# Performance work log

Hardware: AMD Instinct MI355X
Metric: run time of the kernel (lower is better)

Reference implementation:

```python
import jax, jax.numpy as jnp
import numpy as np

K = 9
VOCAB = 7
DIM = 512
LOW = 256  # downsampled bottleneck dim
N_LAYERS = 2
EPS = 1e-5


def _inorm(x, g, b):
    # InstanceNorm1d over length axis (biased var), x: (N, C, K)
    m = jnp.mean(x, axis=-1, keepdims=True)
    v = jnp.mean((x - m) ** 2, axis=-1, keepdims=True)
    return g[None, :, None] * (x - m) * jax.lax.rsqrt(v + EPS) + b[None, :, None]


def _conv5_same(x, w, b):
    # x: (N, C, K), w: (O, C, 5), dilation 1, padding 'same' -> pad 2
    y = jax.lax.conv_general_dilated(
        x, w, window_strides=(1,), padding=[(2, 2)],
        dimension_numbers=('NCH', 'OIH', 'NCH'))
    return y + b[None, :, None]


def _bytenet_layer(x, p):
    (g1, b1, g2, b2, g3, b3, w1, c1b, w2, c2b, w3, c3b) = p
    h = jax.nn.gelu(_inorm(x, g1, b1), approximate=False)
    h = jnp.einsum('nck,oc->nok', h, w1) + c1b[None, :, None]      # 1x1 conv 512->256
    h = jax.nn.gelu(_inorm(h, g2, b2), approximate=False)
    h = _conv5_same(h, w2, c2b)                                     # k=5 conv 256->256
    h = jax.nn.gelu(_inorm(h, g3, b3), approximate=False)
    h = jnp.einsum('nck,oc->nok', h, w3) + c3b[None, :, None]      # 1x1 conv 256->512
    return h + x  # dropout is identity in eval


def setup_inputs() -> dict:
    key = jax.random.key(0)
    ks = jax.random.split(key, 16)
    x = jax.random.randint(ks[0], (8, 2048), 0, VOCAB)
    emb = jax.random.normal(ks[1], (VOCAB, DIM), jnp.float32) * 0.02
    emb = emb.at[6].set(0.0)  # padding_idx=6
    d = {
        'x': x,
        'emb': emb,
        'ln1_w': jnp.ones((N_LAYERS, DIM)), 'ln1_b': jnp.zeros((N_LAYERS, DIM)),
        'ln2_w': jnp.ones((N_LAYERS, LOW)), 'ln2_b': jnp.zeros((N_LAYERS, LOW)),
        'ln3_w': jnp.ones((N_LAYERS, LOW)), 'ln3_b': jnp.zeros((N_LAYERS, LOW)),
        'c1_w': jax.random.normal(ks[2], (N_LAYERS, LOW, DIM), jnp.float32) * 0.02,
        'c1_b': jnp.zeros((N_LAYERS, LOW)),
        'c2_w': jax.random.normal(ks[3], (N_LAYERS, LOW, LOW, 5), jnp.float32) * 0.02,
        'c2_b': jnp.zeros((N_LAYERS, LOW)),
        'c3_w': jax.random.normal(ks[4], (N_LAYERS, DIM, LOW), jnp.float32) * 0.02,
        'c3_b': jnp.zeros((N_LAYERS, DIM)),
        'out_w': jax.random.normal(ks[5], (VOCAB, DIM * K), jnp.float32) * 0.02,
        'out_b': jnp.zeros((VOCAB,)),
    }
    return d


def reference(x, emb, ln1_w, ln1_b, ln2_w, ln2_b, ln3_w, ln3_b,
              c1_w, c1_b, c2_w, c2_b, c3_w, c3_b, out_w, out_b):
    B, L = x.shape
    W = L - K + 1
    e = emb[x]                                        # (B, L, D)
    idx = jnp.arange(W)[:, None] + jnp.arange(K)      # (W, K)
    win = e[:, idx, :]                                # (B, W, K, D)
    h = win.transpose(0, 1, 3, 2).reshape(B * W, DIM, K)  # (N, D, K)
    for i in range(N_LAYERS):
        p = (ln1_w[i], ln1_b[i], ln2_w[i], ln2_b[i], ln3_w[i], ln3_b[i],
             c1_w[i], c1_b[i], c2_w[i], c2_b[i], c3_w[i], c3_b[i])
        h = _bytenet_layer(h, p)
    pred = h.reshape(B * W, DIM * K) @ out_w.T + out_b
    return pred.reshape(B, W, VOCAB)
```

## Files before the change

### kernel.cpp

```cpp
#include <hip/hip_runtime.h>

typedef __attribute__((ext_vector_type(8))) short bfv8;
typedef __attribute__((ext_vector_type(4))) float f32x4;
typedef __attribute__((ext_vector_type(4))) unsigned short usv4;

typedef __attribute__((address_space(1))) const void gvoid;
typedef __attribute__((address_space(3))) void lvoid;
__device__ __forceinline__ void gload16(const void* g, void* l) {
  __builtin_amdgcn_global_load_lds((gvoid*)g, (lvoid*)l, 16, 0, 0);
}

__device__ __forceinline__ float bf2f(unsigned short u) {
  union { unsigned int i; float f; } c; c.i = ((unsigned int)u) << 16; return c.f;
}
__device__ __forceinline__ unsigned short f2bf(float f) {
  union { float f; unsigned int i; } c; c.f = f;
  unsigned int r = c.i + 0x7FFFu + ((c.i >> 16) & 1u);
  return (unsigned short)(r >> 16);
}
__device__ __forceinline__ float gelu_(float x) {
  float z2 = 1.5957691216057308f * x * __builtin_fmaf(0.044715f, x * x, 1.0f);
  float e = __expf(z2);
  float t = __builtin_amdgcn_rcpf(e + 1.0f);
  return x - x * t;
}
__device__ __forceinline__ int div9(int col) {
  return (int)(__umulhi((unsigned)col, 954437177u) >> 1);
}

#define CHP 132

__global__ void k_prep(const float* c1w, const float* c2w, const float* c3w,
                       const float* outw, unsigned short* W1b, unsigned short* W2t,
                       unsigned short* W3b, float* OWt) {
  int i = blockIdx.x * 256 + threadIdx.x;
  if (i < 262144) { W1b[i] = f2bf(c1w[i]); return; }
  i -= 262144;
  if (i < 655360) {
    int ii = i & 255, o = (i >> 8) & 255, rest = i >> 16;
    int t = rest % 5, l = rest / 5;
    W2t[i] = f2bf(c2w[(((l * 256 + o) << 8) + ii) * 5 + t]);
    return;
  }
  i -= 655360;
  if (i < 262144) { W3b[i] = f2bf(c3w[i]); return; }
  i -= 262144;
  if (i < 32256) {
    int c = i & 511, rk = i >> 9;
    int r = rk / 9, k = rk - 9 * r;
    OWt[i] = outw[r * 4608 + c * 9 + k];
  }
}

__global__ void k_x0(const int* x, const float* emb, unsigned short* X, int n0) {
  int idx = blockIdx.x * 256 + threadIdx.x;
  int c4 = idx & 127, nl = idx >> 7;
  int gn = n0 + nl, b = gn >> 11, w = gn & 2047;
  unsigned short* dst = X + (size_t)(12 + nl * 12) * 512 + (c4 << 2);
  const int* xb = x + (b << 11);
  #pragma unroll
  for (int k = 0; k < 9; k++) {
    int t = w + k; if (t > 2047) t = 2047;
    const float* e = emb + xb[t] * 512 + (c4 << 2);
    float4 ev = *(const float4*)e;
    usv4 pk;
    pk[0] = f2bf(ev.x); pk[1] = f2bf(ev.y);
    pk[2] = f2bf(ev.z); pk[3] = f2bf(ev.w);
    *(usv4*)(dst + k * 512) = pk;
  }
}

__global__ void k_zpad(unsigned short* AL) {
  int i = threadIdx.x;
  for (; i < 12 * 256; i += 256) AL[i] = 0;
}

template <int MODE>
__global__ __launch_bounds__(512, 2) void k_gemm(
    const unsigned short* __restrict__ Aw, const unsigned short* __restrict__ Bsrc,
    const float* __restrict__ cbias, const float* __restrict__ n1w,
    const float* __restrict__ n1b, const float* __restrict__ gw,
    const float* __restrict__ gb, unsigned short* __restrict__ Out, int nkc) {
  __shared__ __align__(16) unsigned short smem[69632];
  unsigned short* sE = smem;

  const int KROW = (MODE == 0) ? 512 : 256;
  const int KSTEPS = (MODE == 1) ? 20 : ((MODE == 0) ? 8 : 4);
  int tid = threadIdx.x, wv = tid >> 6, ln = tid & 63;
  int lr = ln >> 3, lu = ln & 7;
  int swz = (lu ^ lr) << 3;
  int m0 = (MODE == 2) ? ((int)blockIdx.y << 8) : 0;
  int w0 = blockIdx.x << 5;
  int col0 = blockIdx.x * 288;

  int brow[5];
  #pragma unroll
  for (int s = 0; s < 5; s++) {
    int colg = col0 + (s << 6) + (wv << 3) + lr;
    if (colg >= nkc) colg = nkc - 1;
    brow[s] = colg + 3 * div9(colg) + 12;
  }
  const unsigned short* A0 = Aw + (size_t)m0 * KROW;

  f32x4 acc[4][9];
  #pragma unroll
  for (int i = 0; i < 4; i++)
    #pragma unroll
    for (int j = 0; j < 9; j++) acc[i][j] = (f32x4){0.f, 0.f, 0.f, 0.f};

  auto stage = [&](int buf, int ks) {
    int kb, dlt; const unsigned short* Ab;
    if (MODE == 1) {
      int t = ks % 5; kb = (ks / 5) << 6; dlt = t - 2; Ab = A0 + t * 65536;
    } else { kb = ks << 6; dlt = 0; Ab = A0; }
    unsigned short* cA = smem + buf * 16384;
    unsigned short* cB = smem + 32768 + buf * 18432;
    #pragma unroll
    for (int p = 0; p < 4; p++) {
      int m = (p << 6) + (wv << 3) + lr;
      gload16(Ab + (size_t)m * KROW + kb + swz, cA + (p << 12) + (wv << 9));
    }
    #pragma unroll
    for (int s = 0; s < 4; s++)
      gload16(Bsrc + (size_t)(brow[s] + dlt) * KROW + kb + swz,
              cB + (s << 12) + (wv << 9));
    if (wv < 4)
      gload16(Bsrc + (size_t)(brow[4] + dlt) * KROW + kb + swz,
              cB + (4 << 12) + (wv << 9));
  };

  stage(0, 0);
  __syncthreads();

  int cur = 0;
  for (int ks = 0; ks < KSTEPS; ks++) {
    unsigned short* cA = smem + cur * 16384;
    unsigned short* cB = smem + 32768 + cur * 18432;

    if (MODE == 0) {
      int cg = tid & 15, win = tid >> 4;
      int u = cg >> 1, sub = (cg & 1) << 3;
      int gch = (ks << 6) + (cg << 2);
      float v[9][4], s1[4] = {0.f, 0.f, 0.f, 0.f};
      #pragma unroll
      for (int k = 0; k < 9; k++) {
        int cl = win * 9 + k;
        usv4 rv = *(const usv4*)((char*)cB + cl * 128 + ((u ^ (cl & 7)) << 4) + sub);
        #pragma unroll
        for (int j = 0; j < 4; j++) { v[k][j] = bf2f(rv[j]); s1[j] += v[k][j]; }
      }
      float mn[4], rr[4], gg[4], bo[4];
      #pragma unroll
      for (int j = 0; j < 4; j++) {
        mn[j] = s1[j] * (1.0f / 9.0f);
        float q = 0.f;
        #pragma unroll
        for (int k = 0; k < 9; k++) { float d = v[k][j] - mn[j]; q += d * d; }
        rr[j] = rsqrtf(q * (1.0f / 9.0f) + 1e-5f);
        gg[j] = n1w[gch + j]; bo[j] = n1b[gch + j];
      }
      #pragma unroll
      for (int k = 0; k < 9; k++) {
        int cl = win * 9 + k;
        usv4 pk;
        #pragma unroll
        for (int j = 0; j < 4; j++)
          pk[j] = f2bf(gelu_(gg[j] * (v[k][j] - mn[j]) * rr[j] + bo[j]));
        *(usv4*)((char*)cB + cl * 128 + ((u ^ (cl & 7)) << 4) + sub) = pk;
      }
      __syncthreads();
    }

    if (ks + 1 < KSTEPS) stage(cur ^ 1, ks + 1);

    int l16 = ln & 15, loct = ln >> 4;
    int wm = wv >> 1, wn = wv & 1;
    #pragma unroll
    for (int kk = 0; kk < 2; kk++) {
      int kbyte = (kk << 6) + (loct << 4);
      bfv8 af[4], bf_[9];
      #pragma unroll
      for (int mi = 0; mi < 4; mi++) {
        int row = (wm << 6) + (mi << 4) + l16;
        af[mi] = *(const bfv8*)((const char*)cA + row * 128 + (kbyte ^ ((row & 7) << 4)));
      }
      #pragma unroll
      for (int ni = 0; ni < 9; ni++) {
        int row = wn * 144 + (ni << 4) + l16;
        bf_[ni] = *(const bfv8*)((const char*)cB + row * 128 + (kbyte ^ ((row & 7) << 4)));
      }
      #pragma unroll
      for (int mi = 0; mi < 4; mi++)
        #pragma unroll
        for (int ni = 0; ni < 9; ni++)
          acc[mi][ni] = __builtin_amdgcn_mfma_f32_16x16x32_bf16(
              af[mi], bf_[ni], acc[mi][ni], 0, 0, 0);
    }
    __syncthreads();
    cur ^= 1;
  }

  int l16 = ln & 15, loct = ln >> 4;
  #pragma unroll
  for (int R = 0; R < 2; R++) {
    if (R) __syncthreads();
    if ((wv >> 2) == R) {
      int chh = (((wv >> 1) & 1) << 6) + (loct << 2);
      int colb = (wv & 1) * 144 + l16;
      #pragma unroll
      for (int mi = 0; mi < 4; mi++) {
        #pragma unroll
        for (int ni = 0; ni < 9; ni++) {
          usv4 pk;
          #pragma unroll
          for (int q = 0; q < 4; q++) pk[q] = f2bf(acc[mi][ni][q]);
          *(usv4*)(sE + (colb + (ni << 4)) * CHP + chh + (mi << 4)) = pk;
        }
      }
    }
    __syncthreads();
    #pragma unroll
    for (int tt = 0; tt < 2; tt++) {
      int t = tid + tt * 512;
      int c4 = t & 31, win = t >> 5;
      int chl = (R << 7) + (c4 << 2);
      const unsigned short* sb = sE + (win * 9) * CHP + (c4 << 2);
      if (MODE == 2) {
        int chg = m0 + chl;
        size_t ob = (size_t)(12 + (size_t)(w0 + win) * 12) * 512 + chg;
        float cb[4];
        #pragma unroll
        for (int j = 0; j < 4; j++) cb[j] = cbias[chg + j];
        #pragma unroll
        for (int k = 0; k < 9; k++) {
          usv4 rv = *(const usv4*)(sb + k * CHP);
          usv4 old = *(usv4*)(Out + ob + k * 512);
          usv4 pk;
          #pragma unroll
          for (int j = 0; j < 4; j++)
            pk[j] = f2bf(bf2f(rv[j]) + cb[j] + bf2f(old[j]));
          *(usv4*)(Out + ob + k * 512) = pk;
        }
      } else {
        size_t ob = (size_t)(12 + (size_t)(w0 + win) * 12) * 256 + chl;
        float s1[4] = {0.f, 0.f, 0.f, 0.f}, s2[4] = {0.f, 0.f, 0.f, 0.f};
        #pragma unroll
        for (int k = 0; k < 9; k++) {
          usv4 rv = *(const usv4*)(sb + k * CHP);
          #pragma unroll
          for (int j = 0; j < 4; j++) {
            float f = bf2f(rv[j]);
            s1[j] += f; s2[j] = __builtin_fmaf(f, f, s2[j]);
          }
        }
        float mn[4], rr[4], gg[4], bo[4];
        #pragma unroll
        for (int j = 0; j < 4; j++) {
          mn[j] = s1[j] * (1.0f / 9.0f);
          float var = s2[j] * (1.0f / 9.0f) - mn[j] * mn[j];
          rr[j] = rsqrtf(var + 1e-5f);
          gg[j] = gw[chl + j]; bo[j] = gb[chl + j];
        }
        #pragma unroll
        for (int k = 0; k < 9; k++) {
          usv4 rv = *(const usv4*)(sb + k * CHP);
          usv4 pk;
          #pragma unroll
          for (int j = 0; j < 4; j++)
            pk[j] = f2bf(gelu_(gg[j] * (bf2f(rv[j]) - mn[j]) * rr[j] + bo[j]));
          *(usv4*)(Out + ob + k * 256) = pk;
        }
        if (MODE == 0) {
          usv4 z = (usv4){0, 0, 0, 0};
          *(usv4*)(Out + ob + 9 * 256) = z;
          *(usv4*)(Out + ob + 10 * 256) = z;
          *(usv4*)(Out + ob + 11 * 256) = z;
        }
      }
    }
  }
}

__global__ void k_out(const unsigned short* X, const float* OWt, const float* outb,
                      float* pred, int n0, int nc) {
  int gw = (blockIdx.x * 256 + threadIdx.x) >> 6;
  int ln = threadIdx.x & 63;
  if (gw >= nc) return;
  int gn = n0 + gw, b = gn >> 11, w = gn & 2047;
  if (w >= 2040) return;
  const unsigned short* xb = X + (size_t)(12 + gw * 12) * 512 + ln * 8;
  float a[7];
  #pragma unroll
  for (int r = 0; r < 7; r++) a[r] = 0.f;
  for (int k = 0; k < 9; k++) {
    bfv8 xv = *(const bfv8*)(xb + k * 512);
    float xf[8];
    #pragma unroll
    for (int j = 0; j < 8; j++) xf[j] = bf2f((unsigned short)xv[j]);
    #pragma unroll
    for (int r = 0; r < 7; r++) {
      const float* wp = OWt + (r * 9 + k) * 512 + ln * 8;
      float4 w0 = *(const float4*)(wp);
      float4 w1 = *(const float4*)(wp + 4);
      a[r] += xf[0] * w0.x + xf[1] * w0.y + xf[2] * w0.z + xf[3] * w0.w +
              xf[4] * w1.x + xf[5] * w1.y + xf[6] * w1.z + xf[7] * w1.w;
    }
  }
  #pragma unroll
  for (int r = 0; r < 7; r++)
    for (int off = 32; off; off >>= 1) a[r] += __shfl_down(a[r], off);
  if (ln == 0) {
    float* o = pred + (size_t)(b * 2040 + w) * 7;
    #pragma unroll
    for (int r = 0; r < 7; r++) o[r] = a[r] + outb[r];
  }
}

extern "C" void kernel_launch(void* const* d_in, const int* in_sizes, int n_in,
                              void* d_out, int out_size, void* d_ws, size_t ws_size,
                              hipStream_t stream) {
  const int*   x    = (const int*)d_in[0];
  const float* emb  = (const float*)d_in[1];
  const float* ln1w = (const float*)d_in[2];
  const float* ln1b = (const float*)d_in[3];
  const float* ln2w = (const float*)d_in[4];
  const float* ln2b = (const float*)d_in[5];
  const float* ln3w = (const float*)d_in[6];
  const float* ln3b = (const float*)d_in[7];
  const float* c1w  = (const float*)d_in[8];
  const float* c2w  = (const float*)d_in[10];
  const float* c3w  = (const float*)d_in[12];
  const float* c3b  = (const float*)d_in[13];
  const float* outw = (const float*)d_in[14];
  const float* outb = (const float*)d_in[15];
  float* pred = (float*)d_out;

  int nc = 8192;
  while (nc > 128 &&
         2488320ull + (unsigned long long)(nc + 1) * 24576ull > ws_size)
    nc >>= 1;
  int nkc = nc * 9;
  int tiles = nc >> 5;
  int nchunks = 16384 / nc;

  char* ws = (char*)d_ws;
  unsigned short* W1b = (unsigned short*)(ws);
  unsigned short* W2t = (unsigned short*)(ws + 524288);
  unsigned short* W3b = (unsigned short*)(ws + 1835008);
  float*          OWt = (float*)(ws + 2359296);
  char* act = ws + 2488320;
  size_t hiB = (size_t)(nc + 1) * 12288;
  size_t loB = (size_t)(nc + 1) * 6144;
  unsigned short* X   = (unsigned short*)(act);
  unsigned short* AL  = (unsigned short*)(act + hiB);
  unsigned short* AL2 = (unsigned short*)(act + hiB + loB);

  k_prep<<<(1211904 + 255) / 256, 256, 0, stream>>>(c1w, c2w, c3w, outw,
                                                    W1b, W2t, W3b, OWt);
  k_zpad<<<1, 256, 0, stream>>>(AL);

  for (int ch = 0; ch < nchunks; ch++) {
    int n0 = ch * nc;
    k_x0<<<nc / 2, 256, 0, stream>>>(x, emb, X, n0);
    for (int l = 0; l < 2; l++) {
      k_gemm<0><<<dim3(tiles, 1), 512, 0, stream>>>(
          W1b + l * 131072, X, nullptr, ln1w + l * 512, ln1b + l * 512,
          ln2w + l * 256, ln2b + l * 256, AL, nkc);
      k_gemm<1><<<dim3(tiles, 1), 512, 0, stream>>>(
          W2t + l * 327680, AL, nullptr, nullptr, nullptr,
          ln3w + l * 256, ln3b + l * 256, AL2, nkc);
      k_gemm<2><<<dim3(tiles, 2), 512, 0, stream>>>(
          W3b + l * 131072, AL2, c3b + l * 512, nullptr, nullptr,
          nullptr, nullptr, X, nkc);
    }
    k_out<<<nc / 4, 256, 0, stream>>>(X, OWt, outb, pred, n0, nc);
  }
}
```

Before: 798.0 us.

## Halve GEMM tile to 256x144 with 256 threads and single-buffered LDS

Shrinks the fused GEMM block tile from 288 columns (32 windows) to 144 columns (16 windows) and from 512 to 256 threads, doubling the grid. It drops the LDS double buffer and stages each k-step synchronously, cutting LDS use from about 136KB to about 50KB so more blocks fit per CU. The epilogue is reworked to four rounds of one wave each. The cost is that global loads no longer overlap with MFMA inside a block, and each block reuses the A tile across fewer columns.

```diff
diff --git a/kernel.cpp b/kernel.cpp
--- a/kernel.cpp
+++ b/kernel.cpp
@@ -28,7 +28,7 @@
   return (int)(__umulhi((unsigned)col, 954437177u) >> 1);
 }
 
-#define CHP 132
+#define CHP 66
 
 __global__ void k_prep(const float* c1w, const float* c2w, const float* c3w,
                        const float* outw, unsigned short* W1b, unsigned short* W2t,
@@ -76,31 +76,34 @@
 }
 
 template <int MODE>
-__global__ __launch_bounds__(512, 2) void k_gemm(
+__global__ __launch_bounds__(256, 2) void k_gemm(
     const unsigned short* __restrict__ Aw, const unsigned short* __restrict__ Bsrc,
     const float* __restrict__ cbias, const float* __restrict__ n1w,
     const float* __restrict__ n1b, const float* __restrict__ gw,
     const float* __restrict__ gb, unsigned short* __restrict__ Out, int nkc) {
-  __shared__ __align__(16) unsigned short smem[69632];
+  __shared__ __align__(16) unsigned short smem[25600];
+  unsigned short* cA = smem;
+  unsigned short* cB = smem + 16384;
   unsigned short* sE = smem;
 
   const int KROW = (MODE == 0) ? 512 : 256;
   const int KSTEPS = (MODE == 1) ? 20 : ((MODE == 0) ? 8 : 4);
   int tid = threadIdx.x, wv = tid >> 6, ln = tid & 63;
   int lr = ln >> 3, lu = ln & 7;
-  int swz = (lu ^ lr) << 3;
   int m0 = (MODE == 2) ? ((int)blockIdx.y << 8) : 0;
-  int w0 = blockIdx.x << 5;
-  int col0 = blockIdx.x * 288;
+  int w0 = blockIdx.x << 4;
+  int col0 = blockIdx.x * 144;
 
   int brow[5];
   #pragma unroll
   for (int s = 0; s < 5; s++) {
-    int colg = col0 + (s << 6) + (wv << 3) + lr;
+    int cl = (s < 4) ? ((s << 5) + (wv << 3) + lr) : (128 + (wv << 3) + lr);
+    int colg = col0 + cl;
     if (colg >= nkc) colg = nkc - 1;
     brow[s] = colg + 3 * div9(colg) + 12;
   }
   const unsigned short* A0 = Aw + (size_t)m0 * KROW;
+  int swz = (lu ^ lr) << 3;
 
   f32x4 acc[4][9];
   #pragma unroll
@@ -108,34 +111,26 @@
     #pragma unroll
     for (int j = 0; j < 9; j++) acc[i][j] = (f32x4){0.f, 0.f, 0.f, 0.f};
 
-  auto stage = [&](int buf, int ks) {
+  for (int ks = 0; ks < KSTEPS; ks++) {
     int kb, dlt; const unsigned short* Ab;
     if (MODE == 1) {
       int t = ks % 5; kb = (ks / 5) << 6; dlt = t - 2; Ab = A0 + t * 65536;
     } else { kb = ks << 6; dlt = 0; Ab = A0; }
-    unsigned short* cA = smem + buf * 16384;
-    unsigned short* cB = smem + 32768 + buf * 18432;
-    #pragma unroll
-    for (int p = 0; p < 4; p++) {
-      int m = (p << 6) + (wv << 3) + lr;
-      gload16(Ab + (size_t)m * KROW + kb + swz, cA + (p << 12) + (wv << 9));
+
+    if (ks) __syncthreads();
+    #pragma unroll
+    for (int p = 0; p < 8; p++) {
+      int m = (p << 5) + (wv << 3) + lr;
+      gload16(Ab + (size_t)m * KROW + kb + swz, cA + ((p << 5) + (wv << 3)) * 64);
     }
     #pragma unroll
     for (int s = 0; s < 4; s++)
       gload16(Bsrc + (size_t)(brow[s] + dlt) * KROW + kb + swz,
-              cB + (s << 12) + (wv << 9));
-    if (wv < 4)
+              cB + ((s << 5) + (wv << 3)) * 64);
+    if (wv < 2)
       gload16(Bsrc + (size_t)(brow[4] + dlt) * KROW + kb + swz,
-              cB + (4 << 12) + (wv << 9));
-  };
-
-  stage(0, 0);
-  __syncthreads();
-
-  int cur = 0;
-  for (int ks = 0; ks < KSTEPS; ks++) {
-    unsigned short* cA = smem + cur * 16384;
-    unsigned short* cB = smem + 32768 + cur * 18432;
+              cB + (128 + (wv << 3)) * 64);
+    __syncthreads();
 
     if (MODE == 0) {
       int cg = tid & 15, win = tid >> 4;
@@ -171,22 +166,19 @@
       __syncthreads();
     }
 
-    if (ks + 1 < KSTEPS) stage(cur ^ 1, ks + 1);
-
     int l16 = ln & 15, loct = ln >> 4;
-    int wm = wv >> 1, wn = wv & 1;
     #pragma unroll
     for (int kk = 0; kk < 2; kk++) {
       int kbyte = (kk << 6) + (loct << 4);
       bfv8 af[4], bf_[9];
       #pragma unroll
       for (int mi = 0; mi < 4; mi++) {
-        int row = (wm << 6) + (mi << 4) + l16;
+        int row = (wv << 6) + (mi << 4) + l16;
         af[mi] = *(const bfv8*)((const char*)cA + row * 128 + (kbyte ^ ((row & 7) << 4)));
       }
       #pragma unroll
       for (int ni = 0; ni < 9; ni++) {
-        int row = wn * 144 + (ni << 4) + l16;
+        int row = (ni << 4) + l16;
         bf_[ni] = *(const bfv8*)((const char*)cB + row * 128 + (kbyte ^ ((row & 7) << 4)));
       }
       #pragma unroll
@@ -196,34 +188,29 @@
           acc[mi][ni] = __builtin_amdgcn_mfma_f32_16x16x32_bf16(
               af[mi], bf_[ni], acc[mi][ni], 0, 0, 0);
     }
+  }
+
+  int l16 = ln & 15, loct = ln >> 4;
+  int c4 = tid & 15, win = tid >> 4;
+  #pragma unroll
+  for (int R = 0; R < 4; R++) {
     __syncthreads();
-    cur ^= 1;
-  }
-
-  int l16 = ln & 15, loct = ln >> 4;
-  #pragma unroll
-  for (int R = 0; R < 2; R++) {
-    if (R) __syncthreads();
-    if ((wv >> 2) == R) {
-      int chh = (((wv >> 1) & 1) << 6) + (loct << 2);
-      int colb = (wv & 1) * 144 + l16;
+    if (wv == R) {
       #pragma unroll
       for (int mi = 0; mi < 4; mi++) {
+        int chh = (mi << 4) + (loct << 2);
         #pragma unroll
         for (int ni = 0; ni < 9; ni++) {
           usv4 pk;
           #pragma unroll
           for (int q = 0; q < 4; q++) pk[q] = f2bf(acc[mi][ni][q]);
-          *(usv4*)(sE + (colb + (ni << 4)) * CHP + chh + (mi << 4)) = pk;
+          *(usv4*)(sE + ((ni << 4) + l16) * CHP + chh) = pk;
         }
       }
     }
     __syncthreads();
-    #pragma unroll
-    for (int tt = 0; tt < 2; tt++) {
-      int t = tid + tt * 512;
-      int c4 = t & 31, win = t >> 5;
-      int chl = (R << 7) + (c4 << 2);
+    {
+      int chl = (R << 6) + (c4 << 2);
       const unsigned short* sb = sE + (win * 9) * CHP + (c4 << 2);
       if (MODE == 2) {
         int chg = m0 + chl;
@@ -340,7 +327,7 @@
          2488320ull + (unsigned long long)(nc + 1) * 24576ull > ws_size)
     nc >>= 1;
   int nkc = nc * 9;
-  int tiles = nc >> 5;
+  int tiles = nc >> 4;
   int nchunks = 16384 / nc;
 
   char* ws = (char*)d_ws;
@@ -363,13 +350,13 @@
     int n0 = ch * nc;
     k_x0<<<nc / 2, 256, 0, stream>>>(x, emb, X, n0);
     for (int l = 0; l < 2; l++) {
-      k_gemm<0><<<dim3(tiles, 1), 512, 0, stream>>>(
+      k_gemm<0><<<dim3(tiles, 1), 256, 0, stream>>>(
           W1b + l * 131072, X, nullptr, ln1w + l * 512, ln1b + l * 512,
           ln2w + l * 256, ln2b + l * 256, AL, nkc);
-      k_gemm<1><<<dim3(tiles, 1), 512, 0, stream>>>(
+      k_gemm<1><<<dim3(tiles, 1), 256, 0, stream>>>(
           W2t + l * 327680, AL, nullptr, nullptr, nullptr,
           ln3w + l * 256, ln3b + l * 256, AL2, nkc);
-      k_gemm<2><<<dim3(tiles, 2), 512, 0, stream>>>(
+      k_gemm<2><<<dim3(tiles, 2), 256, 0, stream>>>(
           W3b + l * 131072, AL2, c3b + l * 512, nullptr, nullptr,
           nullptr, nullptr, X, nkc);
     }
```

Measured after the change: 980.9 us. +22.9%, slower.
